# Kernel optimization log

Hardware: AMD Instinct MI355X
Metric: run time of the kernel (lower is better)

The kernel has to match this reference:

```python
import jax, jax.numpy as jnp
import numpy as np
import math

N, NP, D, H, W, HEADS = 4, 1024, 256, 64, 64, 8
DH = D // HEADS


def _norm_coords(height, width):
    # (height*width, 2) with (x, y) in [0, 1], row-major flatten (y outer, x inner)
    y = jnp.linspace(0.0, 1.0, height)
    x = jnp.linspace(0.0, 1.0, width)
    yg, xg = jnp.meshgrid(y, x, indexing='ij')
    return jnp.stack([xg.reshape(-1), yg.reshape(-1)], axis=-1)


def _pos_enc(coords, dim):
    # coords: (P, 2) -> (P, dim); even slots sin(x*div), odd slots cos(y*div)
    div = jnp.exp(jnp.arange(0, dim, 2, dtype=coords.dtype) * (-math.log(10000.0) / dim))
    s = jnp.sin(coords[:, 0:1] * div)  # (P, dim/2)
    c = jnp.cos(coords[:, 1:2] * div)  # (P, dim/2)
    return jnp.stack([s, c], axis=-1).reshape(coords.shape[0], dim)


def setup_inputs() -> dict:
    key = jax.random.key(0)
    ks = jax.random.split(key, 10)
    sc = 1.0 / math.sqrt(D)
    return {
        "local_feat": jax.random.normal(ks[0], (N, NP, D), jnp.float32),
        "global_feat": jax.random.normal(ks[1], (N, D, H, W), jnp.float32),
        "Wq": jax.random.normal(ks[2], (D, D), jnp.float32) * sc,
        "bq": jax.random.normal(ks[3], (D,), jnp.float32) * sc,
        "Wk": jax.random.normal(ks[4], (D, D), jnp.float32) * sc,
        "bk": jax.random.normal(ks[5], (D,), jnp.float32) * sc,
        "Wv": jax.random.normal(ks[6], (D, D), jnp.float32) * sc,
        "bv": jax.random.normal(ks[7], (D,), jnp.float32) * sc,
        "Wo": jax.random.normal(ks[8], (D, D), jnp.float32) * sc,
        "bo": jax.random.normal(ks[9], (D,), jnp.float32) * sc,
    }


def reference(local_feat, global_feat, Wq, bq, Wk, bk, Wv, bv, Wo, bo):
    n, N_p, d = local_feat.shape
    _, _, h, w = global_feat.shape
    hw = h * w
    P = int(math.sqrt(N_p))

    gf = jnp.transpose(global_feat.reshape(n, d, hw), (0, 2, 1))  # (n, HW, d)

    lf = local_feat + _pos_enc(_norm_coords(P, P), d)[None]       # (n, N_p, d)
    gf = gf + _pos_enc(_norm_coords(h, w), d)[None]               # (n, HW, d)

    q = (lf @ Wq.T + bq).reshape(n, N_p, HEADS, DH)
    k = (gf @ Wk.T + bk).reshape(n, hw, HEADS, DH)
    v = (gf @ Wv.T + bv).reshape(n, hw, HEADS, DH)

    scores = jnp.einsum('bqhd,bkhd->bhqk', q, k) / math.sqrt(DH)  # (n, H, N_p, HW)
    attn = jax.nn.softmax(scores, axis=-1)
    out = jnp.einsum('bhqk,bkhd->bqhd', attn, v).reshape(n, N_p, d)

    return (lf + out) @ Wo.T + bo
```

## Files before the change

kernel.cpp:

```cpp
#include <hip/hip_runtime.h>
#include <hip/hip_bf16.h>
#include <math.h>

#define NB    4
#define NPTS  1024
#define DD    256
#define HWW   4096
#define NHEAD 8
#define DHD   32
#define VTROW 4128

typedef short s8v  __attribute__((ext_vector_type(8)));
typedef float f4v  __attribute__((ext_vector_type(4)));
typedef unsigned int u2v __attribute__((ext_vector_type(2)));
typedef unsigned int u4v __attribute__((ext_vector_type(4)));

#define MFMA_BF16 __builtin_amdgcn_mfma_f32_16x16x32_bf16

#define PE_FACT (-9.210340371976184f / 256.0f)
#define QSCALE 0.2550348637f

__device__ __forceinline__ unsigned packbf(float hi, float lo) {
    return __builtin_amdgcn_perm(__float_as_uint(hi), __float_as_uint(lo), 0x07060302u);
}

__global__ __launch_bounds__(256) void prep(const float* __restrict__ lf,
                                            const float* __restrict__ gfeat,
                                            const float* __restrict__ wq,
                                            const float* __restrict__ wk,
                                            const float* __restrict__ wv,
                                            const float* __restrict__ wo,
                                            __hip_bfloat16* __restrict__ lf_pe_b,
                                            __hip_bfloat16* __restrict__ gf_pe_b,
                                            __hip_bfloat16* __restrict__ W4) {
    __shared__ float tile[32][33];
    int b = blockIdx.x, tid = threadIdx.x;
    if (b < 4096) {
        int idx = b * 256 + tid;
        int c = idx & 255, p = (idx >> 8) & 1023;
        float div = __expf((float)(c & ~1) * PE_FACT);
        float pe = (c & 1) ? __cosf((float)(p >> 5) * (1.0f / 31.0f) * div)
                           : __sinf((float)(p & 31) * (1.0f / 31.0f) * div);
        lf_pe_b[idx] = __float2bfloat16(lf[idx] + pe);
    } else if (b < 8192) {
        int t = b - 4096;
        int n = t >> 10, r = t & 1023;
        int p0 = (r >> 3) * 32, c0 = (r & 7) * 32;
        int tx = tid & 31, ty = tid >> 5;
#pragma unroll
        for (int i = 0; i < 4; ++i)
            tile[ty + 8 * i][tx] = gfeat[((size_t)n * DD + (c0 + ty + 8 * i)) * HWW + p0 + tx];
        __syncthreads();
#pragma unroll
        for (int i = 0; i < 4; ++i) {
            int p = p0 + ty + 8 * i, c = c0 + tx;
            float div = __expf((float)(c & ~1) * PE_FACT);
            float pe = (c & 1) ? __cosf((float)(p >> 6) * (1.0f / 63.0f) * div)
                               : __sinf((float)(p & 63) * (1.0f / 63.0f) * div);
            gf_pe_b[((size_t)n * HWW + p) * DD + c] = __float2bfloat16(tile[tx][ty + 8 * i] + pe);
        }
    } else {
        int idx = (b - 8192) * 256 + tid;
        int m = idx >> 16, r = idx & 65535;
        const float* src = (m == 0) ? wq : (m == 1) ? wk : (m == 2) ? wv : wo;
        W4[idx] = __float2bfloat16(src[r]);
    }
}

__global__ __launch_bounds__(256) void gemmQKV(const __hip_bfloat16* __restrict__ Aq,
                                               const __hip_bfloat16* __restrict__ Akv,
                                               const __hip_bfloat16* __restrict__ W4,
                                               const float* __restrict__ bq,
                                               const float* __restrict__ bk,
                                               const float* __restrict__ bv,
                                               __hip_bfloat16* __restrict__ Qb,
                                               __hip_bfloat16* __restrict__ Kb,
                                               __hip_bfloat16* __restrict__ Vtb) {
    __shared__ __align__(16) unsigned stv[64][36];
    int tid = threadIdx.x;
    int wave = tid >> 6, lane = tid & 63;
    int quad = lane >> 4, c16 = lane & 15;
    int b = blockIdx.x;

    if (b < 256) {
        int m0 = (b & 63) * 64 + wave * 16;
        int c0 = (b >> 6) * 64;
        const short* ap = (const short*)Aq + (m0 + c16) * DD + quad * 8;
        const short* wp = (const short*)W4 + (c0 + c16) * DD + quad * 8;
        f4v acc0 = {0.f,0.f,0.f,0.f}, acc1 = acc0, acc2 = acc0, acc3 = acc0;
#pragma unroll
        for (int ks = 0; ks < 8; ++ks) {
            int o = ks * 32;
            s8v a  = *(const s8v*)(ap + o);
            s8v b0 = *(const s8v*)(wp + o);
            s8v b1 = *(const s8v*)(wp + o + 16 * DD);
            s8v b2 = *(const s8v*)(wp + o + 32 * DD);
            s8v b3 = *(const s8v*)(wp + o + 48 * DD);
            acc0 = MFMA_BF16(a, b0, acc0, 0, 0, 0);
            acc1 = MFMA_BF16(a, b1, acc1, 0, 0, 0);
            acc2 = MFMA_BF16(a, b2, acc2, 0, 0, 0);
            acc3 = MFMA_BF16(a, b3, acc3, 0, 0, 0);
        }
#pragma unroll
        for (int t = 0; t < 4; ++t) {
            f4v acc = (t == 0) ? acc0 : (t == 1) ? acc1 : (t == 2) ? acc2 : acc3;
            int col = c0 + t * 16 + c16;
            float bvv = bq[col];
            int h = col >> 5, dh = col & 31;
#pragma unroll
            for (int r = 0; r < 4; ++r) {
                int row = m0 + quad * 4 + r;
                int n = row >> 10, p = row & 1023;
                Qb[(((size_t)(n * NHEAD + h) << 10) + p) * DHD + dh] =
                    __float2bfloat16((acc[r] + bvv) * QSCALE);
            }
        }
    } else {
        int b2 = b - 256;
        int mblk = b2 & 255;
        int m0 = mblk * 64 + wave * 16;
        int c0 = (b2 >> 8) * 64;
        const short* ap  = (const short*)Akv + (m0 + c16) * DD + quad * 8;
        const short* wkp = (const short*)W4 + DD * DD     + (c0 + c16) * DD + quad * 8;
        const short* wvp = (const short*)W4 + 2 * DD * DD + (c0 + c16) * DD + quad * 8;
        f4v ak0 = {0.f,0.f,0.f,0.f}, ak1 = ak0, ak2 = ak0, ak3 = ak0;
        f4v av0 = ak0, av1 = ak0, av2 = ak0, av3 = ak0;
#pragma unroll
        for (int ks = 0; ks < 8; ++ks) {
            int o = ks * 32;
            s8v a  = *(const s8v*)(ap + o);
            s8v k0 = *(const s8v*)(wkp + o);
            s8v k1 = *(const s8v*)(wkp + o + 16 * DD);
            s8v k2 = *(const s8v*)(wkp + o + 32 * DD);
            s8v k3 = *(const s8v*)(wkp + o + 48 * DD);
            ak0 = MFMA_BF16(a, k0, ak0, 0, 0, 0);
            ak1 = MFMA_BF16(a, k1, ak1, 0, 0, 0);
            ak2 = MFMA_BF16(a, k2, ak2, 0, 0, 0);
            ak3 = MFMA_BF16(a, k3, ak3, 0, 0, 0);
            s8v v0 = *(const s8v*)(wvp + o);
            s8v v1 = *(const s8v*)(wvp + o + 16 * DD);
            s8v v2 = *(const s8v*)(wvp + o + 32 * DD);
            s8v v3 = *(const s8v*)(wvp + o + 48 * DD);
            av0 = MFMA_BF16(a, v0, av0, 0, 0, 0);
            av1 = MFMA_BF16(a, v1, av1, 0, 0, 0);
            av2 = MFMA_BF16(a, v2, av2, 0, 0, 0);
            av3 = MFMA_BF16(a, v3, av3, 0, 0, 0);
        }
        int blkbase = mblk * 64;
        int nblk = blkbase >> 12;
        int kb   = blkbase & 4095;
#pragma unroll
        for (int t = 0; t < 4; ++t) {
            f4v accK = (t == 0) ? ak0 : (t == 1) ? ak1 : (t == 2) ? ak2 : ak3;
            f4v accV = (t == 0) ? av0 : (t == 1) ? av1 : (t == 2) ? av2 : av3;
            int col = c0 + t * 16 + c16;
            float bkv = bk[col], bvv = bv[col];
            int h = col >> 5, dh = col & 31;
#pragma unroll
            for (int r = 0; r < 4; ++r) {
                int row = m0 + quad * 4 + r;
                int p = row & 4095;
                Kb[(((size_t)(nblk * NHEAD + h) << 12) + p) * DHD + dh] =
                    __float2bfloat16(accK[r] + bkv);
            }
#pragma unroll
            for (int rp = 0; rp < 2; ++rp) {
                __hip_bfloat16 lo = __float2bfloat16(accV[2 * rp] + bvv);
                __hip_bfloat16 hi = __float2bfloat16(accV[2 * rp + 1] + bvv);
                unsigned dw = (unsigned)*(unsigned short*)&lo | ((unsigned)*(unsigned short*)&hi << 16);
                stv[t * 16 + c16][wave * 8 + quad * 2 + rp] = dw;
            }
        }
        __syncthreads();
        int col = tid >> 2;
        int kd  = (tid & 3) * 8;
        int grp = kd & 16;
        int ob  = kd & 15;
        unsigned vals[8];
#pragma unroll
        for (int i = 0; i < 8; ++i) {
            int o = ob + i;
            int idw = ((o >> 2) << 1) | (o & 1) | ((o & 2) << 2);
            vals[i] = stv[col][grp + idw];
        }
        u4v w0 = {vals[0], vals[1], vals[2], vals[3]};
        u4v w1 = {vals[4], vals[5], vals[6], vals[7]};
        int gh = (c0 + col) >> 5, gdh = (c0 + col) & 31;
        short* vp = (short*)Vtb + ((size_t)(nblk * NHEAD + gh) * DHD + gdh) * VTROW + kb + kd * 2;
        *(u4v*)(vp)     = w0;
        *(u4v*)(vp + 8) = w1;
    }
}

template <int NC>
__global__ __launch_bounds__(256) void attn(const __hip_bfloat16* __restrict__ Q,
                                            const __hip_bfloat16* __restrict__ Kg,
                                            const __hip_bfloat16* __restrict__ Vt,
                                            __hip_bfloat16* __restrict__ Opart,
                                            float* __restrict__ lpart) {
    constexpr int CK = HWW / NC;
    constexpr int NSTEP = CK / 32;

    int tid = threadIdx.x;
    int wave = tid >> 6, lane = tid & 63;
    int quad = lane >> 4, c16 = lane & 15;

    int id = blockIdx.x;
    int xcd = id & 7;
    int s = id >> 3;
    int qtile = s & 3;
    int gidx = ((s >> 2) << 3) | xcd;
    int bh = gidx & 31;
    int chunk = gidx >> 5;

    int q0 = qtile * 256 + wave * 64;

    const short* Qs = (const short*)Q + (size_t)bh * NPTS * DHD;
    const short* Ks = (const short*)Kg + ((size_t)bh * HWW + (size_t)chunk * CK) * DHD;
    const short* Vs = (const short*)Vt + (size_t)bh * DHD * VTROW + (size_t)chunk * CK;

    s8v aq[4];
#pragma unroll
    for (int g = 0; g < 4; ++g)
        aq[g] = *(const s8v*)(Qs + (q0 + g * 16 + c16) * DHD + quad * 8);

    const f4v zf = {0.f, 0.f, 0.f, 0.f};
    f4v o[4][2];
#pragma unroll
    for (int g = 0; g < 4; ++g) { o[g][0] = zf; o[g][1] = zf; }
    float lsum[4] = {0.f, 0.f, 0.f, 0.f};

    const short* kbase  = Ks + c16 * DHD + quad * 8;
    const short* v0base = Vs + c16 * VTROW + quad * 8;
    const short* v1base = Vs + (16 + c16) * VTROW + quad * 8;

    s8v kfA = *(const s8v*)(kbase);
    s8v kfB = *(const s8v*)(kbase + 16 * DHD);
    s8v vfA = *(const s8v*)(v0base);
    s8v vfB = *(const s8v*)(v1base);

    for (int st = 0; st < NSTEP; ++st) {
        bool more = (st + 1) < NSTEP;
        s8v nkA, nkB, nvA, nvB;
        if (more) {
            int ko = (st + 1) * 32;
            nkA = *(const s8v*)(kbase + ko * DHD);
            nkB = *(const s8v*)(kbase + ko * DHD + 16 * DHD);
            nvA = *(const s8v*)(v0base + ko);
            nvB = *(const s8v*)(v1base + ko);
        }
#pragma unroll
        for (int g = 0; g < 4; ++g) {
            f4v sA = MFMA_BF16(kfA, aq[g], zf, 0, 0, 0);
            f4v sB = MFMA_BF16(kfB, aq[g], zf, 0, 0, 0);
            float pA0 = __builtin_amdgcn_exp2f(sA[0]);
            float pA1 = __builtin_amdgcn_exp2f(sA[1]);
            float pA2 = __builtin_amdgcn_exp2f(sA[2]);
            float pA3 = __builtin_amdgcn_exp2f(sA[3]);
            float pB0 = __builtin_amdgcn_exp2f(sB[0]);
            float pB1 = __builtin_amdgcn_exp2f(sB[1]);
            float pB2 = __builtin_amdgcn_exp2f(sB[2]);
            float pB3 = __builtin_amdgcn_exp2f(sB[3]);
            lsum[g] += ((pA0 + pA1) + (pA2 + pA3)) + ((pB0 + pB1) + (pB2 + pB3));
            union { u4v u; s8v s; } pf;
            pf.u = (u4v){packbf(pA1, pA0), packbf(pA3, pA2),
                         packbf(pB1, pB0), packbf(pB3, pB2)};
            o[g][0] = MFMA_BF16(vfA, pf.s, o[g][0], 0, 0, 0);
            o[g][1] = MFMA_BF16(vfB, pf.s, o[g][1], 0, 0, 0);
        }
        if (more) { kfA = nkA; kfB = nkB; vfA = nvA; vfB = nvB; }
    }

    size_t obase = (size_t)(chunk * 32 + bh) * NPTS;
#pragma unroll
    for (int g = 0; g < 4; ++g) {
        float l = lsum[g];
        l += __shfl_xor(l, 16);
        l += __shfl_xor(l, 32);
        int q = q0 + g * 16 + c16;
        if (quad == 0) lpart[obase + q] = l;
        unsigned d0 = packbf(o[g][0][1], o[g][0][0]);
        unsigned d1 = packbf(o[g][0][3], o[g][0][2]);
        unsigned d2 = packbf(o[g][1][1], o[g][1][0]);
        unsigned d3 = packbf(o[g][1][3], o[g][1][2]);
        unsigned* op = (unsigned*)Opart + (obase + q) * (DHD / 2);
        *(u2v*)(op + 2 * quad)     = (u2v){d0, d1};
        *(u2v*)(op + 8 + 2 * quad) = (u2v){d2, d3};
    }
}

template <int NC>
__global__ __launch_bounds__(256) void combineO(const __hip_bfloat16* __restrict__ Opart,
                                                const float* __restrict__ lpart,
                                                const __hip_bfloat16* __restrict__ lf_pe,
                                                const __hip_bfloat16* __restrict__ Wo4,
                                                const float* __restrict__ bo,
                                                float* __restrict__ out) {
    __shared__ __align__(16) short al[32][264];
    int tid = threadIdx.x;
    int m0 = blockIdx.x * 32;
    {
        int rl = tid >> 3;
        int h  = tid & 7;
        int rg = m0 + rl;
        int n = rg >> 10, q = rg & 1023;
        size_t bhq = ((size_t)(n * NHEAD + h) << 10) + q;
        float l = 0.f;
        float ov[32];
#pragma unroll
        for (int d = 0; d < 32; ++d) ov[d] = 0.f;
#pragma unroll
        for (int ch = 0; ch < NC; ++ch) {
            size_t base = (size_t)ch * 32 * NPTS + bhq;
            l += lpart[base];
            const unsigned* op = (const unsigned*)((const short*)Opart + base * DHD);
#pragma unroll
            for (int dw = 0; dw < 16; ++dw) {
                unsigned u = op[dw];
                ov[2 * dw]     += __uint_as_float(u << 16);
                ov[2 * dw + 1] += __uint_as_float(u & 0xffff0000u);
            }
        }
        float linv = 1.0f / l;
        const unsigned* lp = (const unsigned*)((const short*)lf_pe + ((size_t)rg * DD + h * 32));
        unsigned* dst = (unsigned*)&al[rl][h * 32];
#pragma unroll
        for (int dw = 0; dw < 16; ++dw) {
            unsigned u = lp[dw];
            float x0 = ov[2 * dw] * linv     + __uint_as_float(u << 16);
            float x1 = ov[2 * dw + 1] * linv + __uint_as_float(u & 0xffff0000u);
            dst[dw] = packbf(x1, x0);
        }
    }
    __syncthreads();
    int wave = tid >> 6, lane = tid & 63;
    int quad = lane >> 4, c16 = lane & 15;
    int rw  = (wave & 1) * 16;
    int ch0 = (wave >> 1) * 128;
    f4v acc[8];
#pragma unroll
    for (int t = 0; t < 8; ++t) acc[t] = (f4v){0.f, 0.f, 0.f, 0.f};
#pragma unroll
    for (int ks = 0; ks < 8; ++ks) {
        s8v af = *(const s8v*)&al[rw + c16][ks * 32 + quad * 8];
#pragma unroll
        for (int t = 0; t < 8; ++t) {
            const short* wp = (const short*)Wo4 + (ch0 + t * 16 + c16) * DD + ks * 32 + quad * 8;
            s8v bf = *(const s8v*)wp;
            acc[t] = MFMA_BF16(af, bf, acc[t], 0, 0, 0);
        }
    }
#pragma unroll
    for (int t = 0; t < 8; ++t) {
        int col = ch0 + t * 16 + c16;
        float bv = bo[col];
#pragma unroll
        for (int r = 0; r < 4; ++r) {
            int row = m0 + rw + quad * 4 + r;
            out[(size_t)row * DD + col] = acc[t][r] + bv;
        }
    }
}

extern "C" void kernel_launch(void* const* d_in, const int* in_sizes, int n_in,
                              void* d_out, int out_size, void* d_ws, size_t ws_size,
                              hipStream_t stream) {
    const float* lf    = (const float*)d_in[0];
    const float* gfeat = (const float*)d_in[1];
    const float* Wq    = (const float*)d_in[2];
    const float* bq    = (const float*)d_in[3];
    const float* Wk    = (const float*)d_in[4];
    const float* bk    = (const float*)d_in[5];
    const float* Wv    = (const float*)d_in[6];
    const float* bv    = (const float*)d_in[7];
    const float* Wo    = (const float*)d_in[8];
    const float* bo    = (const float*)d_in[9];

    const size_t MB = 1u << 20;
    char* ws = (char*)d_ws;
    __hip_bfloat16* lf_pe_b = (__hip_bfloat16*)(ws);
    __hip_bfloat16* gf_pe_b = (__hip_bfloat16*)(ws + 2 * MB);
    __hip_bfloat16* W4      = (__hip_bfloat16*)(ws + 10 * MB);
    __hip_bfloat16* Qb      = (__hip_bfloat16*)(ws + 10 * MB + 512 * 1024);
    __hip_bfloat16* Kb      = (__hip_bfloat16*)(ws + 12 * MB + 512 * 1024);
    __hip_bfloat16* Vtb     = (__hip_bfloat16*)(ws + 20 * MB + 512 * 1024);
    float*          lpart   = (float*)(ws + 31 * MB);
    __hip_bfloat16* Opart   = (__hip_bfloat16*)(ws + 32 * MB);

    prep<<<dim3(9216), dim3(256), 0, stream>>>(lf, gfeat, Wq, Wk, Wv, Wo,
                                               lf_pe_b, gf_pe_b, W4);
    gemmQKV<<<dim3(1280), dim3(256), 0, stream>>>(lf_pe_b, gf_pe_b, W4, bq, bk, bv,
                                                  Qb, Kb, Vtb);

    if (ws_size >= 48 * MB) {
        attn<8><<<dim3(128 * 8), dim3(256), 0, stream>>>(Qb, Kb, Vtb, Opart, lpart);
        combineO<8><<<dim3(128), dim3(256), 0, stream>>>(Opart, lpart, lf_pe_b,
                                                         W4 + 3 * DD * DD, bo, (float*)d_out);
    } else if (ws_size >= 40 * MB) {
        attn<4><<<dim3(128 * 4), dim3(256), 0, stream>>>(Qb, Kb, Vtb, Opart, lpart);
        combineO<4><<<dim3(128), dim3(256), 0, stream>>>(Opart, lpart, lf_pe_b,
                                                         W4 + 3 * DD * DD, bo, (float*)d_out);
    } else if (ws_size >= 36 * MB) {
        attn<2><<<dim3(128 * 2), dim3(256), 0, stream>>>(Qb, Kb, Vtb, Opart, lpart);
        combineO<2><<<dim3(128), dim3(256), 0, stream>>>(Opart, lpart, lf_pe_b,
                                                         W4 + 3 * DD * DD, bo, (float*)d_out);
    } else {
        attn<1><<<dim3(128 * 1), dim3(256), 0, stream>>>(Qb, Kb, Vtb, Opart, lpart);
        combineO<1><<<dim3(128), dim3(256), 0, stream>>>(Opart, lpart, lf_pe_b,
                                                         W4 + 3 * DD * DD, bo, (float*)d_out);
    }
}
```

Before: 177.1 us.

## Restructure QKV GEMM to keep weight tiles in registers across two row tiles

The QKV projection kernel now splits K and V into separate blocks. Each block preloads its 64-column weight slice into registers once and reuses it for two 64-row tiles, which cuts repeated weight reloads and changes the grid from 1280 to 1152 blocks. The launch bound is raised to two blocks per SM. The trade-off is much higher register pressure from 32 weight vectors per thread and less parallelism per block, and the activation rows for K and V are now read twice.

```diff
diff --git a/kernel.cpp b/kernel.cpp
--- a/kernel.cpp
+++ b/kernel.cpp
@@ -67,128 +67,128 @@
     }
 }
 
-__global__ __launch_bounds__(256) void gemmQKV(const __hip_bfloat16* __restrict__ Aq,
-                                               const __hip_bfloat16* __restrict__ Akv,
-                                               const __hip_bfloat16* __restrict__ W4,
-                                               const float* __restrict__ bq,
-                                               const float* __restrict__ bk,
-                                               const float* __restrict__ bv,
-                                               __hip_bfloat16* __restrict__ Qb,
-                                               __hip_bfloat16* __restrict__ Kb,
-                                               __hip_bfloat16* __restrict__ Vtb) {
+__global__ __launch_bounds__(256, 2) void gemmQKV(const __hip_bfloat16* __restrict__ Aq,
+                                                  const __hip_bfloat16* __restrict__ Akv,
+                                                  const __hip_bfloat16* __restrict__ W4,
+                                                  const float* __restrict__ bq,
+                                                  const float* __restrict__ bk,
+                                                  const float* __restrict__ bv,
+                                                  __hip_bfloat16* __restrict__ Qb,
+                                                  __hip_bfloat16* __restrict__ Kb,
+                                                  __hip_bfloat16* __restrict__ Vtb) {
     __shared__ __align__(16) unsigned stv[64][36];
     int tid = threadIdx.x;
     int wave = tid >> 6, lane = tid & 63;
     int quad = lane >> 4, c16 = lane & 15;
     int b = blockIdx.x;
 
-    if (b < 256) {
-        int m0 = (b & 63) * 64 + wave * 16;
-        int c0 = (b >> 6) * 64;
-        const short* ap = (const short*)Aq + (m0 + c16) * DD + quad * 8;
-        const short* wp = (const short*)W4 + (c0 + c16) * DD + quad * 8;
-        f4v acc0 = {0.f,0.f,0.f,0.f}, acc1 = acc0, acc2 = acc0, acc3 = acc0;
+    int typ, c0, mgrp, mstride;
+    const short* Ap;
+    const short* Wp;
+    const float* bias;
+    if (b < 128) {
+        typ = 0; c0 = (b >> 5) * 64; mgrp = b & 31; mstride = 2048;
+        Ap = (const short*)Aq; Wp = (const short*)W4; bias = bq;
+    } else {
+        int bb = b - 128;
+        int combo = bb >> 7;
+        mgrp = bb & 127; mstride = 8192;
+        int mat = combo & 1;
+        typ = 1 + mat;
+        c0 = (combo >> 1) * 64;
+        Ap = (const short*)Akv;
+        Wp = (const short*)W4 + (1 + mat) * DD * DD;
+        bias = mat ? bv : bk;
+    }
+
+    s8v w[8][4];
+    const short* wp0 = Wp + (c0 + c16) * DD + quad * 8;
+#pragma unroll
+    for (int ks = 0; ks < 8; ++ks)
+#pragma unroll
+        for (int t = 0; t < 4; ++t)
+            w[ks][t] = *(const s8v*)(wp0 + t * 16 * DD + ks * 32);
+    float bvv[4];
+#pragma unroll
+    for (int t = 0; t < 4; ++t) bvv[t] = bias[c0 + t * 16 + c16];
+
+#pragma unroll
+    for (int it = 0; it < 2; ++it) {
+        int mbase = mgrp * 64 + it * mstride;
+        int m0 = mbase + wave * 16;
+        const short* ap = Ap + (m0 + c16) * DD + quad * 8;
+        s8v a[8];
+#pragma unroll
+        for (int ks = 0; ks < 8; ++ks) a[ks] = *(const s8v*)(ap + ks * 32);
+
+        f4v acc[4];
+#pragma unroll
+        for (int t = 0; t < 4; ++t) acc[t] = (f4v){0.f, 0.f, 0.f, 0.f};
 #pragma unroll
         for (int ks = 0; ks < 8; ++ks) {
-            int o = ks * 32;
-            s8v a  = *(const s8v*)(ap + o);
-            s8v b0 = *(const s8v*)(wp + o);
-            s8v b1 = *(const s8v*)(wp + o + 16 * DD);
-            s8v b2 = *(const s8v*)(wp + o + 32 * DD);
-            s8v b3 = *(const s8v*)(wp + o + 48 * DD);
-            acc0 = MFMA_BF16(a, b0, acc0, 0, 0, 0);
-            acc1 = MFMA_BF16(a, b1, acc1, 0, 0, 0);
-            acc2 = MFMA_BF16(a, b2, acc2, 0, 0, 0);
-            acc3 = MFMA_BF16(a, b3, acc3, 0, 0, 0);
-        }
-#pragma unroll
-        for (int t = 0; t < 4; ++t) {
-            f4v acc = (t == 0) ? acc0 : (t == 1) ? acc1 : (t == 2) ? acc2 : acc3;
-            int col = c0 + t * 16 + c16;
-            float bvv = bq[col];
-            int h = col >> 5, dh = col & 31;
-#pragma unroll
-            for (int r = 0; r < 4; ++r) {
-                int row = m0 + quad * 4 + r;
-                int n = row >> 10, p = row & 1023;
-                Qb[(((size_t)(n * NHEAD + h) << 10) + p) * DHD + dh] =
-                    __float2bfloat16((acc[r] + bvv) * QSCALE);
+#pragma unroll
+            for (int t = 0; t < 4; ++t)
+                acc[t] = MFMA_BF16(a[ks], w[ks][t], acc[t], 0, 0, 0);
+        }
+
+        if (typ == 0) {
+#pragma unroll
+            for (int t = 0; t < 4; ++t) {
+                int col = c0 + t * 16 + c16;
+                int h = col >> 5, dh = col & 31;
+#pragma unroll
+                for (int r = 0; r < 4; ++r) {
+                    int row = m0 + quad * 4 + r;
+                    int n = row >> 10, p = row & 1023;
+                    Qb[(((size_t)(n * NHEAD + h) << 10) + p) * DHD + dh] =
+                        __float2bfloat16((acc[t][r] + bvv[t]) * QSCALE);
+                }
             }
-        }
-    } else {
-        int b2 = b - 256;
-        int mblk = b2 & 255;
-        int m0 = mblk * 64 + wave * 16;
-        int c0 = (b2 >> 8) * 64;
-        const short* ap  = (const short*)Akv + (m0 + c16) * DD + quad * 8;
-        const short* wkp = (const short*)W4 + DD * DD     + (c0 + c16) * DD + quad * 8;
-        const short* wvp = (const short*)W4 + 2 * DD * DD + (c0 + c16) * DD + quad * 8;
-        f4v ak0 = {0.f,0.f,0.f,0.f}, ak1 = ak0, ak2 = ak0, ak3 = ak0;
-        f4v av0 = ak0, av1 = ak0, av2 = ak0, av3 = ak0;
-#pragma unroll
-        for (int ks = 0; ks < 8; ++ks) {
-            int o = ks * 32;
-            s8v a  = *(const s8v*)(ap + o);
-            s8v k0 = *(const s8v*)(wkp + o);
-            s8v k1 = *(const s8v*)(wkp + o + 16 * DD);
-            s8v k2 = *(const s8v*)(wkp + o + 32 * DD);
-            s8v k3 = *(const s8v*)(wkp + o + 48 * DD);
-            ak0 = MFMA_BF16(a, k0, ak0, 0, 0, 0);
-            ak1 = MFMA_BF16(a, k1, ak1, 0, 0, 0);
-            ak2 = MFMA_BF16(a, k2, ak2, 0, 0, 0);
-            ak3 = MFMA_BF16(a, k3, ak3, 0, 0, 0);
-            s8v v0 = *(const s8v*)(wvp + o);
-            s8v v1 = *(const s8v*)(wvp + o + 16 * DD);
-            s8v v2 = *(const s8v*)(wvp + o + 32 * DD);
-            s8v v3 = *(const s8v*)(wvp + o + 48 * DD);
-            av0 = MFMA_BF16(a, v0, av0, 0, 0, 0);
-            av1 = MFMA_BF16(a, v1, av1, 0, 0, 0);
-            av2 = MFMA_BF16(a, v2, av2, 0, 0, 0);
-            av3 = MFMA_BF16(a, v3, av3, 0, 0, 0);
-        }
-        int blkbase = mblk * 64;
-        int nblk = blkbase >> 12;
-        int kb   = blkbase & 4095;
-#pragma unroll
-        for (int t = 0; t < 4; ++t) {
-            f4v accK = (t == 0) ? ak0 : (t == 1) ? ak1 : (t == 2) ? ak2 : ak3;
-            f4v accV = (t == 0) ? av0 : (t == 1) ? av1 : (t == 2) ? av2 : av3;
-            int col = c0 + t * 16 + c16;
-            float bkv = bk[col], bvv = bv[col];
-            int h = col >> 5, dh = col & 31;
-#pragma unroll
-            for (int r = 0; r < 4; ++r) {
-                int row = m0 + quad * 4 + r;
-                int p = row & 4095;
-                Kb[(((size_t)(nblk * NHEAD + h) << 12) + p) * DHD + dh] =
-                    __float2bfloat16(accK[r] + bkv);
+        } else if (typ == 1) {
+#pragma unroll
+            for (int t = 0; t < 4; ++t) {
+                int col = c0 + t * 16 + c16;
+                int h = col >> 5, dh = col & 31;
+#pragma unroll
+                for (int r = 0; r < 4; ++r) {
+                    int row = m0 + quad * 4 + r;
+                    int n = row >> 12, p = row & 4095;
+                    Kb[(((size_t)(n * NHEAD + h) << 12) + p) * DHD + dh] =
+                        __float2bfloat16(acc[t][r] + bvv[t]);
+                }
             }
-#pragma unroll
-            for (int rp = 0; rp < 2; ++rp) {
-                __hip_bfloat16 lo = __float2bfloat16(accV[2 * rp] + bvv);
-                __hip_bfloat16 hi = __float2bfloat16(accV[2 * rp + 1] + bvv);
-                unsigned dw = (unsigned)*(unsigned short*)&lo | ((unsigned)*(unsigned short*)&hi << 16);
-                stv[t * 16 + c16][wave * 8 + quad * 2 + rp] = dw;
+        } else {
+            __syncthreads();
+#pragma unroll
+            for (int t = 0; t < 4; ++t) {
+#pragma unroll
+                for (int rp = 0; rp < 2; ++rp) {
+                    __hip_bfloat16 lo = __float2bfloat16(acc[t][2 * rp] + bvv[t]);
+                    __hip_bfloat16 hi = __float2bfloat16(acc[t][2 * rp + 1] + bvv[t]);
+                    unsigned dw = (unsigned)*(unsigned short*)&lo |
+                                  ((unsigned)*(unsigned short*)&hi << 16);
+                    stv[t * 16 + c16][wave * 8 + quad * 2 + rp] = dw;
+                }
             }
-        }
-        __syncthreads();
-        int col = tid >> 2;
-        int kd  = (tid & 3) * 8;
-        int grp = kd & 16;
-        int ob  = kd & 15;
-        unsigned vals[8];
-#pragma unroll
-        for (int i = 0; i < 8; ++i) {
-            int o = ob + i;
-            int idw = ((o >> 2) << 1) | (o & 1) | ((o & 2) << 2);
-            vals[i] = stv[col][grp + idw];
-        }
-        u4v w0 = {vals[0], vals[1], vals[2], vals[3]};
-        u4v w1 = {vals[4], vals[5], vals[6], vals[7]};
-        int gh = (c0 + col) >> 5, gdh = (c0 + col) & 31;
-        short* vp = (short*)Vtb + ((size_t)(nblk * NHEAD + gh) * DHD + gdh) * VTROW + kb + kd * 2;
-        *(u4v*)(vp)     = w0;
-        *(u4v*)(vp + 8) = w1;
+            __syncthreads();
+            int col = tid >> 2;
+            int kd  = (tid & 3) * 8;
+            int grp = kd & 16;
+            int ob  = kd & 15;
+            unsigned vals[8];
+#pragma unroll
+            for (int i = 0; i < 8; ++i) {
+                int o = ob + i;
+                int idw = ((o >> 2) << 1) | (o & 1) | ((o & 2) << 2);
+                vals[i] = stv[col][grp + idw];
+            }
+            int nblk = mbase >> 12;
+            int kb   = mbase & 4095;
+            int gh = (c0 + col) >> 5, gdh = (c0 + col) & 31;
+            short* vp = (short*)Vtb + ((size_t)(nblk * NHEAD + gh) * DHD + gdh) * VTROW + kb + kd * 2;
+            *(u4v*)(vp)     = (u4v){vals[0], vals[1], vals[2], vals[3]};
+            *(u4v*)(vp + 8) = (u4v){vals[4], vals[5], vals[6], vals[7]};
+        }
     }
 }
 
@@ -389,7 +389,7 @@
 
     prep<<<dim3(9216), dim3(256), 0, stream>>>(lf, gfeat, Wq, Wk, Wv, Wo,
                                                lf_pe_b, gf_pe_b, W4);
-    gemmQKV<<<dim3(1280), dim3(256), 0, stream>>>(lf_pe_b, gf_pe_b, W4, bq, bk, bv,
+    gemmQKV<<<dim3(1152), dim3(256), 0, stream>>>(lf_pe_b, gf_pe_b, W4, bq, bk, bv,
                                                   Qb, Kb, Vtb);
 
     if (ws_size >= 48 * MB) {
```

Measured after the change: 168.7 us. 1.05x faster.
